# Kernel tuning notes

Measured on AMD Instinct MI355X. Metric: run time of the kernel, lower is better.

## Reference

```python
import jax, jax.numpy as jnp
import numpy as np

# CrossAttention (DFFNet): 1x1 convs produce q,k from depth and v from rgb;
# full dense attention over hw spatial tokens: softmax(q^T k) then v @ mask^T.

def setup_inputs() -> dict:
    key = jax.random.key(0)
    ks = jax.random.split(key, 8)
    B, C, H, W = 4, 256, 64, 64
    Cqk = C // 8  # ratio=8 -> 32
    s = 0.02
    return {
        "rgb":   jax.random.normal(ks[0], (B, C, H, W), jnp.float32),
        "depth": jax.random.normal(ks[1], (B, C, H, W), jnp.float32),
        "Wq": jax.random.normal(ks[2], (Cqk, C), jnp.float32) * s,
        "bq": jax.random.normal(ks[3], (Cqk,), jnp.float32) * s,
        "Wk": jax.random.normal(ks[4], (Cqk, C), jnp.float32) * s,
        "bk": jax.random.normal(ks[5], (Cqk,), jnp.float32) * s,
        "Wv": jax.random.normal(ks[6], (C, C), jnp.float32) * s,
        "bv": jax.random.normal(ks[7], (C,), jnp.float32) * s,
    }


def reference(rgb, depth, Wq, bq, Wk, bk, Wv, bv):
    B, C, H, W = rgb.shape
    hw = H * W
    d = depth.reshape(B, C, hw)   # [B, C, hw]
    r = rgb.reshape(B, C, hw)     # [B, C, hw]
    # 1x1 convs == channel-mixing linear maps
    q = jnp.einsum('oc,bcn->bon', Wq, d) + bq[None, :, None]  # [B, Cqk, hw]
    k = jnp.einsum('oc,bcn->bon', Wk, d) + bk[None, :, None]  # [B, Cqk, hw]
    v = jnp.einsum('oc,bcn->bon', Wv, r) + bv[None, :, None]  # [B, C, hw]
    # scores: q^T k -> [B, hw, hw], softmax over last dim
    scores = jnp.einsum('bcn,bcm->bnm', q, k)
    mask = jax.nn.softmax(scores, axis=-1)
    # feat = v @ mask^T  -> [B, C, hw]
    feat = jnp.einsum('bcm,bnm->bcn', v, mask)
    return feat.reshape(B, C, H, W)
```

## Files before the change

### kernel.cpp

```cpp
#include <hip/hip_runtime.h>
#include <stdint.h>

#define L2E 1.44269504088896340736f

typedef _Float16 half8 __attribute__((ext_vector_type(8)));
typedef float floatx4 __attribute__((ext_vector_type(4)));

static __device__ __forceinline__ unsigned short f32_to_f16u(float f) {
  union { _Float16 h; unsigned short s; } cv; cv.h = (_Float16)f; return cv.s;
}

typedef __attribute__((address_space(3))) unsigned int as3_uint;
typedef __attribute__((address_space(1))) const unsigned int as1_cuint;

static __device__ __forceinline__ void async16(const void* g, void* l) {
  __builtin_amdgcn_global_load_lds((as1_cuint*)g, (as3_uint*)l, 16, 0, 0);
}

__global__ __launch_bounds__(256) void proj_kernel(
    const float* __restrict__ rgb,
    const float* __restrict__ depth,
    const float* __restrict__ Wq, const float* __restrict__ bq,
    const float* __restrict__ Wk, const float* __restrict__ bk,
    const float* __restrict__ Wv, const float* __restrict__ bv,
    unsigned short* __restrict__ qT,
    unsigned short* __restrict__ kT,
    unsigned short* __restrict__ v)
{
  __shared__ __align__(16) unsigned short sW[64 * 256];

  const int n0 = blockIdx.x * 64;
  const int b  = blockIdx.y;
  const int z  = blockIdx.z;
  const int t  = threadIdx.x;
  const int w  = t >> 6;
  const int lane = t & 63;
  const int l15 = lane & 15;
  const int q4  = lane >> 4;

  const float* X = (z == 0) ? depth : rgb;
  const float* xb = X + (size_t)b * 256 * 4096;
  const int n_row = n0 + 16 * w + l15;

  half8 a8[8];
#pragma unroll
  for (int ks = 0; ks < 8; ks++) {
#pragma unroll
    for (int j = 0; j < 8; j++) {
      int c = ks * 32 + q4 * 8 + j;
      a8[ks][j] = (_Float16)xb[(size_t)c * 4096 + n_row];
    }
  }

  const int nq = (z == 0) ? 1 : 2;
  for (int qd = 0; qd < nq; qd++) {
    const int colbase = (z == 0) ? 0 : (z - 1) * 128 + qd * 64;
    __syncthreads();

#pragma unroll
    for (int it = 0; it < 8; it++) {
      int L = it * 256 + t;
      int og = L >> 5;
      int phys = L & 31;
      int ci = phys ^ (og & 7);
      const float* wr;
      if (z == 0) wr = (og < 32) ? (Wq + (size_t)og * 256) : (Wk + (size_t)(og - 32) * 256);
      else        wr = Wv + (size_t)(colbase + og) * 256;
      float4 w0 = *(const float4*)(wr + ci * 8);
      float4 w1 = *(const float4*)(wr + ci * 8 + 4);
      half8 h;
      h[0] = (_Float16)w0.x; h[1] = (_Float16)w0.y; h[2] = (_Float16)w0.z; h[3] = (_Float16)w0.w;
      h[4] = (_Float16)w1.x; h[5] = (_Float16)w1.y; h[6] = (_Float16)w1.z; h[7] = (_Float16)w1.w;
      *(half8*)&sW[(size_t)L * 8] = h;
    }

    float bias[4];
#pragma unroll
    for (int ct = 0; ct < 4; ct++) {
      int og = ct * 16 + l15;
      if (z == 0) bias[ct] = (og < 32) ? bq[og] : bk[og - 32];
      else        bias[ct] = bv[colbase + og];
    }
    __syncthreads();

    floatx4 acc[4];
#pragma unroll
    for (int i = 0; i < 4; i++) acc[i] = (floatx4){0.f, 0.f, 0.f, 0.f};

#pragma unroll
    for (int ks = 0; ks < 8; ks++) {
      const int ci = ks * 4 + q4;
#pragma unroll
      for (int ct = 0; ct < 4; ct++) {
        int og = ct * 16 + l15;
        half8 bf = *(const half8*)&sW[og * 256 + ((ci ^ (og & 7)) * 8)];
        acc[ct] = __builtin_amdgcn_mfma_f32_16x16x32_f16(a8[ks], bf, acc[ct], 0, 0, 0);
      }
    }

    __syncthreads();

    if (z == 0) {
#pragma unroll
      for (int ct = 0; ct < 4; ct++) {
        int og = ct * 16 + l15;
#pragma unroll
        for (int r = 0; r < 4; r++) {
          int n = n0 + 16 * w + q4 * 4 + r;
          unsigned short hv = f32_to_f16u(acc[ct][r] + bias[ct]);
          if (og < 32) qT[((size_t)b * 4096 + n) * 32 + og] = hv;
          else         kT[((size_t)b * 4096 + n) * 32 + (og - 32)] = hv;
        }
      }
    } else {
      unsigned short* tile = sW;
#pragma unroll
      for (int ct = 0; ct < 4; ct++) {
#pragma unroll
        for (int r = 0; r < 4; r++) {
          int co_l = ct * 16 + l15;
          int nl = 16 * w + q4 * 4 + r;
          tile[co_l * 72 + nl] = f32_to_f16u(acc[ct][r] + bias[ct]);
        }
      }
      __syncthreads();
#pragma unroll
      for (int it = 0; it < 2; it++) {
        int co_l = it * 32 + (t >> 3);
        int ch = t & 7;
        int4 val = *(const int4*)&tile[co_l * 72 + ch * 8];
        *(int4*)&v[((size_t)b * 256 + colbase + co_l) * 4096 + n0 + ch * 8] = val;
      }
    }
  }
}

static __device__ __forceinline__ void stage_v(
    const unsigned short* __restrict__ vB, unsigned char* sbase,
    int m0, int t, int w)
{
#pragma unroll
  for (int j = 0; j < 4; j++) {
    int lin = j * 256 + t;
    int c = lin >> 2;
    int p = lin & 3;
    int lc = p ^ ((c >> 1) & 3);
    async16(&vB[(size_t)c * 4096 + m0 + lc * 8], sbase + j * 4096 + w * 1024);
  }
}

__global__ __launch_bounds__(256, 4) void attn_kernel(
    const unsigned short* __restrict__ qT,
    const unsigned short* __restrict__ kT,
    const unsigned short* __restrict__ v,
    unsigned short* __restrict__ Op,
    float* __restrict__ lW)
{
  __shared__ __align__(16) unsigned char smem[37888];
  unsigned short* sP = (unsigned short*)(smem + 32768);

  const int n0 = blockIdx.x * 64;
  const int b  = blockIdx.y;
  const int chunk = blockIdx.z;
  const int t  = threadIdx.x;
  const int w  = t >> 6;
  const int lane = t & 63;
  const int l15 = lane & 15;
  const int q4  = lane >> 4;

  half8 aq = *(const half8*)(qT + ((size_t)b * 4096 + n0 + 16 * w + l15) * 32 + q4 * 8);

  const unsigned short* vB = v + (size_t)b * 256 * 4096;
  const unsigned short* kL = kT + (size_t)b * 4096 * 32 + (size_t)l15 * 32 + q4 * 8;
  unsigned short* sPw = sP + w * 640;

  float lsum[4] = {0.f, 0.f, 0.f, 0.f};
  floatx4 acc[16];
#pragma unroll
  for (int ct = 0; ct < 16; ct++) acc[ct] = (floatx4){0.f, 0.f, 0.f, 0.f};
  const floatx4 zf = (floatx4){0.f, 0.f, 0.f, 0.f};

  const int mbase = chunk * 1024;

  stage_v(vB, smem, mbase, t, w);
  half8 kc0 = *(const half8*)(kL + (size_t)mbase * 32);
  half8 kc1 = *(const half8*)(kL + (size_t)(mbase + 16) * 32);

  int bufoff = 0;
  for (int it = 0; it < 32; ++it) {
    const int m0 = mbase + it * 32;
    half8 kn0 = kc0, kn1 = kc1;
    if (it < 31) {
      stage_v(vB, smem + (bufoff ^ 16384), m0 + 32, t, w);
      kn0 = *(const half8*)(kL + (size_t)(m0 + 32) * 32);
      kn1 = *(const half8*)(kL + (size_t)(m0 + 48) * 32);
      asm volatile("s_waitcnt vmcnt(6)" ::: "memory");
    } else {
      asm volatile("s_waitcnt vmcnt(0)" ::: "memory");
    }

    floatx4 s0 = __builtin_amdgcn_mfma_f32_16x16x32_f16(aq, kc0, zf, 0, 0, 0);
    floatx4 s1 = __builtin_amdgcn_mfma_f32_16x16x32_f16(aq, kc1, zf, 0, 0, 0);

    float p0[4], p1[4];
#pragma unroll
    for (int r = 0; r < 4; r++) {
      p0[r] = exp2f(s0[r] * L2E);
      p1[r] = exp2f(s1[r] * L2E);
      lsum[r] += p0[r] + p1[r];
    }
#pragma unroll
    for (int r = 0; r < 4; r++) {
      int row = q4 * 4 + r;
      sPw[row * 40 + l15]      = f32_to_f16u(p0[r]);
      sPw[row * 40 + 16 + l15] = f32_to_f16u(p1[r]);
    }
    asm volatile("s_waitcnt lgkmcnt(0)" ::: "memory");

    __builtin_amdgcn_s_barrier();
    asm volatile("s_waitcnt lgkmcnt(0)" ::: "memory");

    half8 ap[4];
#pragma unroll
    for (int nt = 0; nt < 4; nt++)
      ap[nt] = *(const half8*)&sP[nt * 640 + l15 * 40 + q4 * 8];

    const unsigned short* sVb = (const unsigned short*)(smem + bufoff);
#pragma unroll
    for (int ct = 0; ct < 4; ct++) {
      int co = w * 64 + ct * 16 + l15;
      half8 bv8 = *(const half8*)&sVb[co * 32 + ((q4 ^ ((co >> 1) & 3)) * 8)];
#pragma unroll
      for (int nt = 0; nt < 4; nt++)
        acc[ct * 4 + nt] = __builtin_amdgcn_mfma_f32_16x16x32_f16(ap[nt], bv8, acc[ct * 4 + nt], 0, 0, 0);
    }
    asm volatile("s_waitcnt lgkmcnt(0)" ::: "memory");
    __builtin_amdgcn_s_barrier();

    kc0 = kn0; kc1 = kn1;
    bufoff ^= 16384;
  }

#pragma unroll
  for (int off = 1; off < 16; off <<= 1) {
#pragma unroll
    for (int r = 0; r < 4; r++) lsum[r] += __shfl_xor(lsum[r], off);
  }
  if (l15 == 0) {
#pragma unroll
    for (int r = 0; r < 4; r++)
      lW[((size_t)chunk * 4 + b) * 4096 + n0 + 16 * w + q4 * 4 + r] = lsum[r];
  }

  unsigned short* sO = (unsigned short*)smem;
#pragma unroll
  for (int pass = 0; pass < 2; pass++) {
    __syncthreads();
    if ((w >> 1) == pass) {
#pragma unroll
      for (int ct = 0; ct < 4; ct++) {
        int co_l = (w & 1) * 64 + ct * 16 + l15;
#pragma unroll
        for (int nt = 0; nt < 4; nt++) {
#pragma unroll
          for (int r = 0; r < 4; r++) {
            int nl = nt * 16 + q4 * 4 + r;
            sO[co_l * 72 + nl] = f32_to_f16u(acc[ct * 4 + nt][r]);
          }
        }
      }
    }
    __syncthreads();
#pragma unroll
    for (int s = 0; s < 4; s++) {
      int co_l = s * 32 + (t >> 3);
      int ch = t & 7;
      int4 val = *(const int4*)&sO[co_l * 72 + ch * 8];
      *(int4*)&Op[(((size_t)chunk * 4 + b) * 256 + pass * 128 + co_l) * 4096 + n0 + ch * 8] = val;
    }
  }
}

__global__ __launch_bounds__(256) void combine_kernel(
    const unsigned short* __restrict__ Op,
    const float* __restrict__ lW,
    float* __restrict__ out)
{
  const int t = threadIdx.x;
  const int b = blockIdx.y;
  const size_t n8 = (size_t)blockIdx.x * 2048 + (size_t)t * 8;
  const int co0 = blockIdx.z * 8;

  float sum[8] = {0.f, 0.f, 0.f, 0.f, 0.f, 0.f, 0.f, 0.f};
#pragma unroll
  for (int ch = 0; ch < 4; ch++) {
    const float* lp = lW + ((size_t)ch * 4 + b) * 4096 + n8;
    float4 a0 = *(const float4*)lp;
    float4 a1 = *(const float4*)(lp + 4);
    sum[0] += a0.x; sum[1] += a0.y; sum[2] += a0.z; sum[3] += a0.w;
    sum[4] += a1.x; sum[5] += a1.y; sum[6] += a1.z; sum[7] += a1.w;
  }
  float rl[8];
#pragma unroll
  for (int i = 0; i < 8; i++) rl[i] = 1.0f / sum[i];

#pragma unroll
  for (int cc = 0; cc < 8; cc++) {
    int co = co0 + cc;
    float o[8] = {0.f, 0.f, 0.f, 0.f, 0.f, 0.f, 0.f, 0.f};
#pragma unroll
    for (int ch = 0; ch < 4; ch++) {
      half8 hv = *(const half8*)&Op[(((size_t)ch * 4 + b) * 256 + co) * 4096 + n8];
#pragma unroll
      for (int i = 0; i < 8; i++) o[i] += (float)hv[i];
    }
    float* op = out + ((size_t)b * 256 + co) * 4096 + n8;
    float4 r0, r1;
    r0.x = o[0] * rl[0]; r0.y = o[1] * rl[1]; r0.z = o[2] * rl[2]; r0.w = o[3] * rl[3];
    r1.x = o[4] * rl[4]; r1.y = o[5] * rl[5]; r1.z = o[6] * rl[6]; r1.w = o[7] * rl[7];
    *(float4*)op = r0;
    *(float4*)(op + 4) = r1;
  }
}

extern "C" void kernel_launch(void* const* d_in, const int* in_sizes, int n_in,
                              void* d_out, int out_size, void* d_ws, size_t ws_size,
                              hipStream_t stream) {
  const float* rgb   = (const float*)d_in[0];
  const float* depth = (const float*)d_in[1];
  const float* Wq    = (const float*)d_in[2];
  const float* bq    = (const float*)d_in[3];
  const float* Wk    = (const float*)d_in[4];
  const float* bk    = (const float*)d_in[5];
  const float* Wv    = (const float*)d_in[6];
  const float* bv    = (const float*)d_in[7];
  float* out = (float*)d_out;

  unsigned short* qT = (unsigned short*)d_ws;
  unsigned short* kT = qT + (size_t)4 * 4096 * 32;
  unsigned short* vW = kT + (size_t)4 * 4096 * 32;
  unsigned short* Op = vW + (size_t)4 * 256 * 4096;
  float* lW = (float*)(Op + (size_t)4 * 4 * 256 * 4096);

  dim3 pg(64, 4, 3);
  proj_kernel<<<pg, 256, 0, stream>>>(rgb, depth, Wq, bq, Wk, bk, Wv, bv, qT, kT, vW);
  dim3 ag(64, 4, 4);
  attn_kernel<<<ag, 256, 0, stream>>>(qT, kT, vW, Op, lW);
  dim3 cg(2, 4, 32);
  combine_kernel<<<cg, 256, 0, stream>>>(Op, lW, out);
}
```

Before: 163.5 us.

## Stage projection inputs via LDS, remap attention grid, use raw v_exp, split combine

```diff
diff --git a/kernel.cpp b/kernel.cpp
--- a/kernel.cpp
+++ b/kernel.cpp
@@ -8,6 +8,12 @@
 
 static __device__ __forceinline__ unsigned short f32_to_f16u(float f) {
   union { _Float16 h; unsigned short s; } cv; cv.h = (_Float16)f; return cv.s;
+}
+
+static __device__ __forceinline__ float fast_exp2(float x) {
+  float r;
+  asm("v_exp_f32 %0, %1" : "=v"(r) : "v"(x));
+  return r;
 }
 
 typedef __attribute__((address_space(3))) unsigned int as3_uint;
@@ -27,7 +33,8 @@
     unsigned short* __restrict__ kT,
     unsigned short* __restrict__ v)
 {
-  __shared__ __align__(16) unsigned short sW[64 * 256];
+  __shared__ __align__(16) unsigned short sX[256 * 76];
+  __shared__ __align__(16) unsigned short sW[32 * 256];
 
   const int n0 = blockIdx.x * 64;
   const int b  = blockIdx.y;
@@ -39,32 +46,44 @@
   const int q4  = lane >> 4;
 
   const float* X = (z == 0) ? depth : rgb;
-  const float* xb = X + (size_t)b * 256 * 4096;
-  const int n_row = n0 + 16 * w + l15;
+  const float* xb = X + (size_t)b * 256 * 4096 + n0;
+
+#pragma unroll
+  for (int i = 0; i < 8; i++) {
+    int h = i * 256 + t;
+    int c = h >> 3, oct = h & 7;
+    const float* src = xb + (size_t)c * 4096 + oct * 8;
+    float4 x0 = *(const float4*)src;
+    float4 x1 = *(const float4*)(src + 4);
+    half8 hh;
+    hh[0] = (_Float16)x0.x; hh[1] = (_Float16)x0.y; hh[2] = (_Float16)x0.z; hh[3] = (_Float16)x0.w;
+    hh[4] = (_Float16)x1.x; hh[5] = (_Float16)x1.y; hh[6] = (_Float16)x1.z; hh[7] = (_Float16)x1.w;
+    *(half8*)&sX[c * 76 + oct * 8] = hh;
+  }
+  __syncthreads();
 
   half8 a8[8];
 #pragma unroll
   for (int ks = 0; ks < 8; ks++) {
 #pragma unroll
     for (int j = 0; j < 8; j++) {
-      int c = ks * 32 + q4 * 8 + j;
-      a8[ks][j] = (_Float16)xb[(size_t)c * 4096 + n_row];
-    }
-  }
-
-  const int nq = (z == 0) ? 1 : 2;
-  for (int qd = 0; qd < nq; qd++) {
-    const int colbase = (z == 0) ? 0 : (z - 1) * 128 + qd * 64;
-    __syncthreads();
-
-#pragma unroll
-    for (int it = 0; it < 8; it++) {
-      int L = it * 256 + t;
+      a8[ks][j] = *(const _Float16*)&sX[(ks * 32 + q4 * 8 + j) * 76 + 16 * w + l15];
+    }
+  }
+
+  const int ns = (z == 0) ? 2 : 4;
+  for (int s = 0; s < ns; s++) {
+    const int colbase = (z == 0) ? 0 : (z - 1) * 128 + s * 32;
+    __syncthreads();
+
+#pragma unroll
+    for (int i = 0; i < 4; i++) {
+      int L = i * 256 + t;
       int og = L >> 5;
       int phys = L & 31;
       int ci = phys ^ (og & 7);
       const float* wr;
-      if (z == 0) wr = (og < 32) ? (Wq + (size_t)og * 256) : (Wk + (size_t)(og - 32) * 256);
+      if (z == 0) wr = ((s == 0) ? Wq : Wk) + (size_t)og * 256;
       else        wr = Wv + (size_t)(colbase + og) * 256;
       float4 w0 = *(const float4*)(wr + ci * 8);
       float4 w1 = *(const float4*)(wr + ci * 8 + 4);
@@ -74,27 +93,27 @@
       *(half8*)&sW[(size_t)L * 8] = h;
     }
 
-    float bias[4];
-#pragma unroll
-    for (int ct = 0; ct < 4; ct++) {
+    float bias2[2];
+#pragma unroll
+    for (int ct = 0; ct < 2; ct++) {
       int og = ct * 16 + l15;
-      if (z == 0) bias[ct] = (og < 32) ? bq[og] : bk[og - 32];
-      else        bias[ct] = bv[colbase + og];
-    }
-    __syncthreads();
-
-    floatx4 acc[4];
-#pragma unroll
-    for (int i = 0; i < 4; i++) acc[i] = (floatx4){0.f, 0.f, 0.f, 0.f};
+      if (z == 0) bias2[ct] = (s == 0) ? bq[og] : bk[og];
+      else        bias2[ct] = bv[colbase + og];
+    }
+    __syncthreads();
+
+    floatx4 acc2[2];
+    acc2[0] = (floatx4){0.f, 0.f, 0.f, 0.f};
+    acc2[1] = (floatx4){0.f, 0.f, 0.f, 0.f};
 
 #pragma unroll
     for (int ks = 0; ks < 8; ks++) {
       const int ci = ks * 4 + q4;
 #pragma unroll
-      for (int ct = 0; ct < 4; ct++) {
+      for (int ct = 0; ct < 2; ct++) {
         int og = ct * 16 + l15;
         half8 bf = *(const half8*)&sW[og * 256 + ((ci ^ (og & 7)) * 8)];
-        acc[ct] = __builtin_amdgcn_mfma_f32_16x16x32_f16(a8[ks], bf, acc[ct], 0, 0, 0);
+        acc2[ct] = __builtin_amdgcn_mfma_f32_16x16x32_f16(a8[ks], bf, acc2[ct], 0, 0, 0);
       }
     }
 
@@ -102,31 +121,30 @@
 
     if (z == 0) {
 #pragma unroll
-      for (int ct = 0; ct < 4; ct++) {
+      for (int ct = 0; ct < 2; ct++) {
         int og = ct * 16 + l15;
 #pragma unroll
         for (int r = 0; r < 4; r++) {
           int n = n0 + 16 * w + q4 * 4 + r;
-          unsigned short hv = f32_to_f16u(acc[ct][r] + bias[ct]);
-          if (og < 32) qT[((size_t)b * 4096 + n) * 32 + og] = hv;
-          else         kT[((size_t)b * 4096 + n) * 32 + (og - 32)] = hv;
+          unsigned short hv = f32_to_f16u(acc2[ct][r] + bias2[ct]);
+          if (s == 0) qT[((size_t)b * 4096 + n) * 32 + og] = hv;
+          else        kT[((size_t)b * 4096 + n) * 32 + og] = hv;
         }
       }
     } else {
       unsigned short* tile = sW;
 #pragma unroll
-      for (int ct = 0; ct < 4; ct++) {
+      for (int ct = 0; ct < 2; ct++) {
 #pragma unroll
         for (int r = 0; r < 4; r++) {
           int co_l = ct * 16 + l15;
           int nl = 16 * w + q4 * 4 + r;
-          tile[co_l * 72 + nl] = f32_to_f16u(acc[ct][r] + bias[ct]);
+          tile[co_l * 72 + nl] = f32_to_f16u(acc2[ct][r] + bias2[ct]);
         }
       }
       __syncthreads();
-#pragma unroll
-      for (int it = 0; it < 2; it++) {
-        int co_l = it * 32 + (t >> 3);
+      {
+        int co_l = t >> 3;
         int ch = t & 7;
         int4 val = *(const int4*)&tile[co_l * 72 + ch * 8];
         *(int4*)&v[((size_t)b * 256 + colbase + co_l) * 4096 + n0 + ch * 8] = val;
@@ -159,9 +177,11 @@
   __shared__ __align__(16) unsigned char smem[37888];
   unsigned short* sP = (unsigned short*)(smem + 32768);
 
-  const int n0 = blockIdx.x * 64;
-  const int b  = blockIdx.y;
-  const int chunk = blockIdx.z;
+  const int o = blockIdx.x;
+  const int n0 = ((o >> 3) & 63) * 64;
+  const int p  = (o & 7) | ((o >> 9) << 3);
+  const int b  = p & 3;
+  const int chunk = p >> 2;
   const int t  = threadIdx.x;
   const int w  = t >> 6;
   const int lane = t & 63;
@@ -205,8 +225,8 @@
     float p0[4], p1[4];
 #pragma unroll
     for (int r = 0; r < 4; r++) {
-      p0[r] = exp2f(s0[r] * L2E);
-      p1[r] = exp2f(s1[r] * L2E);
+      p0[r] = fast_exp2(s0[r] * L2E);
+      p1[r] = fast_exp2(s1[r] * L2E);
       lsum[r] += p0[r] + p1[r];
     }
 #pragma unroll
@@ -289,7 +309,7 @@
   const int t = threadIdx.x;
   const int b = blockIdx.y;
   const size_t n8 = (size_t)blockIdx.x * 2048 + (size_t)t * 8;
-  const int co0 = blockIdx.z * 8;
+  const int co0 = blockIdx.z * 4;
 
   float sum[8] = {0.f, 0.f, 0.f, 0.f, 0.f, 0.f, 0.f, 0.f};
 #pragma unroll
@@ -305,7 +325,7 @@
   for (int i = 0; i < 8; i++) rl[i] = 1.0f / sum[i];
 
 #pragma unroll
-  for (int cc = 0; cc < 8; cc++) {
+  for (int cc = 0; cc < 4; cc++) {
     int co = co0 + cc;
     float o[8] = {0.f, 0.f, 0.f, 0.f, 0.f, 0.f, 0.f, 0.f};
 #pragma unroll
@@ -344,8 +364,7 @@
 
   dim3 pg(64, 4, 3);
   proj_kernel<<<pg, 256, 0, stream>>>(rgb, depth, Wq, bq, Wk, bk, Wv, bv, qT, kT, vW);
-  dim3 ag(64, 4, 4);
-  attn_kernel<<<ag, 256, 0, stream>>>(qT, kT, vW, Op, lW);
-  dim3 cg(2, 4, 32);
+  attn_kernel<<<dim3(1024, 1, 1), 256, 0, stream>>>(qT, kT, vW, Op, lW);
+  dim3 cg(2, 4, 64);
   combine_kernel<<<cg, 256, 0, stream>>>(Op, lW, out);
 }
```

Result: no change. 160.3 us, median of 2 (-1.9%).
